# Optimization experiments

Hardware: AMD Instinct MI355X
Metric: run time of the kernel (lower is better)

Reference implementation:

```python
import jax, jax.numpy as jnp
import numpy as np

GRID = (8192, 8192)   # 2D lattice, *dims
NDIM = 2              # links.shape[0]
P_LINK = 0.45         # subcritical bond probability -> finite clusters, bounded step count


def setup_inputs() -> dict:
    key = jax.random.key(0)
    k1, k2 = jax.random.split(key)
    # links[i] marks an open bond between site x and its +1 neighbour along axis i
    links = jax.random.uniform(k1, (NDIM,) + GRID) < P_LINK
    seed_idx = jax.random.randint(k2, (NDIM,), 0, GRID[0]).astype(jnp.int32)
    return {"links": links, "seed_idx": seed_idx}


def _flood_fill(links, seed_idx):
    """Faithful port of ClusterSelection.from_seed_idx: BFS-style roll+mask
    expansion iterated to fixed point via lax.while_loop."""
    ndim = links.shape[0]
    grid = links.shape[1:]
    selected0 = jnp.zeros(grid, dtype=bool).at[tuple(seed_idx)].set(True)

    def cond(carry):
        _, is_done, _ = carry
        return ~is_done

    def body(carry):
        sel0, _, steps = carry
        sel = sel0
        for i in range(ndim):  # unrolled over the (small, static) ndim
            # sites whose -1-neighbour or self is selected can use bond i
            links_to_try = sel0 | jnp.roll(sel0, -1, i)
            links_sel = links_to_try & links[i]
            # a taken bond marks both of its endpoints
            links_sel = links_sel | jnp.roll(links_sel, 1, i)
            sel = sel | links_sel
        is_done = (sel ^ sel0).sum() == 0
        return sel, is_done, steps + 1

    sel, _, steps = jax.lax.while_loop(
        cond, body, (selected0, jnp.array(False), jnp.array(0, jnp.int32))
    )
    return sel, steps


def reference(links, seed_idx):
    sel, _steps = _flood_fill(links, seed_idx)
    return sel
```

## Files before the change

kernel.cpp:

```cpp
#include <hip/hip_runtime.h>
#include <stdint.h>

#define GW 8192
#define GMASK 8191
#define PLANE 67108864ULL
#define TPD 128
#define TMASK 127
#define NTILES 16384
#define QCAP 16384
#define QMASK 16383
#define WPR 128

#define WS_BITMAP 4096
#define WS_TFEVER (WS_BITMAP + 8388608)

#define OUT_U4 16777216u

typedef unsigned long long u64;
typedef unsigned int u32;
typedef unsigned int u32x4 __attribute__((ext_vector_type(4)));

__global__ void clear_bitmap_kernel(uint4* __restrict__ p, int n) {
    int i = blockIdx.x * blockDim.x + threadIdx.x;
    if (i < n) p[i] = make_uint4(0, 0, 0, 0);
}

__device__ __forceinline__ u32 nib4(u32 w) {
    return (((w & 0x01010101u) * 0x01020408u) >> 24) & 0xFu;
}
__device__ __forceinline__ u64 pack_row_b8(const unsigned char* p) {
    const uint4* q = (const uint4*)p;
    u64 w = 0;
#pragma unroll
    for (int i = 0; i < 4; i++) {
        uint4 v = q[i];
        u64 nb = (u64)(nib4(v.x) | (nib4(v.y) << 4) | (nib4(v.z) << 8) | (nib4(v.w) << 12));
        w |= nb << (16 * i);
    }
    return w;
}
__device__ __forceinline__ u64 pack_row_b32(const u32* p) {
    u64 w = 0;
#pragma unroll
    for (int k = 0; k < 16; k++) {
        uint4 v = ((const uint4*)p)[k];
        u64 nb = (u64)((v.x != 0) | ((v.y != 0) << 1) | ((v.z != 0) << 2) | ((v.w != 0) << 3));
        w |= nb << (4 * k);
    }
    return w;
}

__global__ void __launch_bounds__(1024)
mega_kernel(const unsigned char* __restrict__ links8,
            const int* __restrict__ seed_idx,
            unsigned char* __restrict__ ws,
            u32x4* __restrict__ outv) {
    volatile __shared__ unsigned short q[QCAP];
    __shared__ u32 tflags[NTILES / 32];
    __shared__ u32 tfever[NTILES / 32];
    __shared__ int s_qhead, s_qtail, s_active, s_mode, s_c1, s_c3;

    if (blockIdx.x != 0) {
        u32 gtid = (blockIdx.x - 1) * 1024 + threadIdx.x;
        u32 stride = (gridDim.x - 1) * 1024;
        u32x4 z = (u32x4)(0u);
        for (u32 i = gtid; i < OUT_U4; i += stride)
            __builtin_nontemporal_store(z, &outv[i]);
        return;
    }

    u64* bitmap = (u64*)(ws + WS_BITMAP);
    const int tid = threadIdx.x;
    const int ln  = tid & 63;

    for (int i = tid; i < QCAP; i += 1024) q[i] = 0xFFFF;
    for (int i = tid; i < NTILES / 32; i += 1024) { tflags[i] = 0; tfever[i] = 0; }
    if (tid == 0) { s_c1 = 0; s_c3 = 0; s_qhead = 0; s_qtail = 0; s_active = 0; }
    __syncthreads();

    int l1c = 0, l3c = 0;
    for (int i = tid; i < 16384; i += 1024) {
        if (links8[i]) { int m = i & 3; if (m == 1) l1c++; else if (m == 3) l3c++; }
    }
    atomicAdd(&s_c1, l1c);
    atomicAdd(&s_c3, l3c);
    __syncthreads();
    if (tid == 0) {
        s_mode = (s_c1 > 0) ? 0 : ((s_c3 > 0) ? 2 : 1);
        int sr = seed_idx[0] & GMASK, sc = seed_idx[1] & GMASK;
        atomicOr(&bitmap[(u64)sr * WPR + (sc >> 6)], 1ull << (sc & 63));
        int t = (sr >> 6) * TPD + (sc >> 6);
        tflags[t >> 5] = 1u << (t & 31);
        tfever[t >> 5] = 1u << (t & 31);
        q[0] = (unsigned short)t;
        s_qtail = 1; s_active = 1;
    }
    __syncthreads();

    const int mode = s_mode;
    const unsigned char* p0b = links8;
    const unsigned char* p1b = links8 + PLANE;
    const u32* p0w = (const u32*)links8;
    const u32* p1w = (const u32*)(links8 + PLANE * 4);

    auto enq = [&](int t2) {
        u32 bit = 1u << (t2 & 31);
        atomicOr(&tfever[t2 >> 5], bit);
        u32 old = atomicOr(&tflags[t2 >> 5], bit);
        if (!(old & bit)) {
            atomicAdd(&s_active, 1);
            int pos = atomicAdd(&s_qtail, 1) & QMASK;
            q[pos] = (unsigned short)t2;
        }
    };

    long long guard = 0;
    while (true) {
        int t = -1;
        if (ln == 0) {
            while (true) {
                if (*(volatile int*)&s_active == 0) break;
                int h  = *(volatile int*)&s_qhead;
                int tl = *(volatile int*)&s_qtail;
                if (h != tl) {
                    if (atomicCAS(&s_qhead, h, h + 1) == h) {
                        int pos = h & QMASK;
                        unsigned short v;
                        long long g2 = 0;
                        while ((v = q[pos]) == 0xFFFF) { if (++g2 > 400000000LL) break; }
                        q[pos] = 0xFFFF;
                        t = v;
                        break;
                    }
                } else {
                    __builtin_amdgcn_s_sleep(1);
                }
                if (++guard > 400000000LL) break;
            }
        }
        t = __shfl(t, 0);
        if (t < 0) break;

        const int tR = t >> 7, tC = t & TMASK;
        const int c0 = tC * 64;
        if (ln == 0) atomicAnd(&tflags[t >> 5], ~(1u << (t & 31)));
        __threadfence_block();

        const int gr = tR * 64 + ln;
        u64* wp = &bitmap[(u64)gr * WPR + tC];
        u64 loaded = *(volatile u64*)wp;

        u64 l0, l1;
        if (mode == 0) {
            l0 = pack_row_b8(p0b + (u64)gr * GW + tC * 64);
            l1 = pack_row_b8(p1b + (u64)gr * GW + tC * 64);
        } else {
            l0 = pack_row_b32(p0w + (u64)gr * GW + tC * 64);
            l1 = pack_row_b32(p1w + (u64)gr * GW + tC * 64);
        }

        u64 P0 = l1 & 0x7FFFFFFFFFFFFFFFull;
        u64 P1 = P0 & (P0 >> 1);
        u64 P2 = P1 & (P1 >> 2);
        u64 P3 = P2 & (P2 >> 4);
        u64 P4 = P3 & (P3 >> 8);
        u64 P5 = P4 & (P4 >> 16);
        u64 D0 = (ln < 63) ? l0 : 0ull;
        u64 D1 = D0 & __shfl_down(D0, 1);
        u64 D2 = D1 & __shfl_down(D1, 2);
        u64 D3 = D2 & __shfl_down(D2, 4);
        u64 D4 = D3 & __shfl_down(D3, 8);
        u64 D5 = D4 & __shfl_down(D4, 16);

        u64 sel = loaded;
        while (true) {
            u64 old = sel;
            sel |= (sel & P0) << 1;  sel |= (sel >> 1)  & P0;
            sel |= (sel & P1) << 2;  sel |= (sel >> 2)  & P1;
            sel |= (sel & P2) << 4;  sel |= (sel >> 4)  & P2;
            sel |= (sel & P3) << 8;  sel |= (sel >> 8)  & P3;
            sel |= (sel & P4) << 16; sel |= (sel >> 16) & P4;
            sel |= (sel & P5) << 32; sel |= (sel >> 32) & P5;
            sel |= __shfl_up(sel & D0, 1);  sel |= __shfl_down(sel, 1)  & D0;
            sel |= __shfl_up(sel & D1, 2);  sel |= __shfl_down(sel, 2)  & D1;
            sel |= __shfl_up(sel & D2, 4);  sel |= __shfl_down(sel, 4)  & D2;
            sel |= __shfl_up(sel & D3, 8);  sel |= __shfl_down(sel, 8)  & D3;
            sel |= __shfl_up(sel & D4, 16); sel |= __shfl_down(sel, 16) & D4;
            sel |= __shfl_up(sel & D5, 32); sel |= __shfl_down(sel, 32) & D5;
            if (__ballot(sel != old) == 0ull) break;
        }

        u64 newbits = sel & ~loaded;
        if (newbits) atomicOr(wp, newbits);

        bool rnew = false, lnew = false;
        if ((sel >> 63) & (l1 >> 63) & 1ull) {
            u64 old = atomicOr(&bitmap[(u64)gr * WPR + ((tC + 1) & TMASK)], 1ull);
            rnew = !(old & 1ull);
        }
        if (sel & 1ull) {
            u64 lcol2 = (u64)((c0 - 1) & GMASK);
            bool lopen = (mode == 0) ? (p1b[(u64)gr * GW + lcol2] != 0)
                                     : (p1w[(u64)gr * GW + lcol2] != 0);
            if (lopen) {
                u64 old = atomicOr(&bitmap[(u64)gr * WPR + ((tC - 1) & TMASK)], 1ull << 63);
                lnew = !(old & (1ull << 63));
            }
        }
        u64 rmask = __ballot(rnew), lmask = __ballot(lnew);

        const int ga = (tR * 64 - 1) & GMASK;
        u64 top_sel = __shfl(sel, 0);
        u64 umask = 0;
        if (top_sel) {
            bool bopen = ((top_sel >> ln) & 1) &&
                ((mode == 0) ? (p0b[(u64)ga * GW + c0 + ln] != 0)
                             : (p0w[(u64)ga * GW + c0 + ln] != 0));
            umask = __ballot(bopen);
        }
        u64 unew = 0;
        if (ln == 0 && umask) {
            u64 old = atomicOr(&bitmap[(u64)ga * WPR + tC], umask);
            unew = umask & ~old;
        }
        u64 dmask = sel & l0;
        const int gb = (tR * 64 + 64) & GMASK;
        u64 dnew = 0;
        if (ln == 63 && dmask) {
            u64 old = atomicOr(&bitmap[(u64)gb * WPR + tC], dmask);
            dnew = dmask & ~old;
        }

        if (ln == 0  && rmask) enq(tR * TPD + ((tC + 1) & TMASK));
        if (ln == 1  && lmask) enq(tR * TPD + ((tC - 1) & TMASK));
        if (ln == 0  && unew)  enq(((tR - 1) & TMASK) * TPD + tC);
        if (ln == 63 && dnew)  enq(((tR + 1) & TMASK) * TPD + tC);

        if (ln == 0) atomicSub(&s_active, 1);
    }

    __syncthreads();
    for (int i = tid; i < NTILES / 32; i += 1024)
        ((u32*)(ws + WS_TFEVER))[i] = tfever[i];
}

__global__ void __launch_bounds__(256)
writeout_sparse(const unsigned char* __restrict__ ws, u32x4* __restrict__ ob) {
    const u64* bitmap = (const u64*)(ws + WS_BITMAP);
    const u32* tf = (const u32*)(ws + WS_TFEVER);
    for (int t = blockIdx.x; t < NTILES; t += gridDim.x) {
        if (!((tf[t >> 5] >> (t & 31)) & 1u)) continue;
        int tR = t >> 7, tC = t & TMASK;
        for (int i = threadIdx.x; i < 1024; i += 256) {
            int row = i >> 4, c4 = i & 15;
            u64 w = bitmap[(u64)(tR * 64 + row) * WPR + tC];
            u32 nb = (u32)(w >> (c4 * 4)) & 0xFu;
            u32x4 v;
            v.x = nb & 1; v.y = (nb >> 1) & 1; v.z = (nb >> 2) & 1; v.w = (nb >> 3) & 1;
            __builtin_nontemporal_store(
                v, &ob[(u64)(tR * 64 + row) * 2048 + tC * 16 + c4]);
        }
    }
}

extern "C" void kernel_launch(void* const* d_in, const int* in_sizes, int n_in,
                              void* d_out, int out_size, void* d_ws, size_t ws_size,
                              hipStream_t stream) {
    const unsigned char* links = (const unsigned char*)d_in[0];
    const int* seed = (const int*)d_in[1];
    unsigned char* ws = (unsigned char*)d_ws;

    u64* bitmap = (u64*)(ws + WS_BITMAP);

    clear_bitmap_kernel<<<2048, 256, 0, stream>>>((uint4*)bitmap, 524288);
    mega_kernel<<<256, 1024, 0, stream>>>(links, seed, ws, (u32x4*)d_out);
    writeout_sparse<<<1024, 256, 0, stream>>>(ws, (u32x4*)d_out);
}
```

Measured before the change: 658.2 us.

## Fuse sparse writeout into mega kernel with grid-level completion counter

Removes the separate writeout_sparse launch. Block 0 now writes the selected tiles itself after spinning on a global counter that the zero-fill blocks increment once their stores are done. The fill grid doubles to 512 blocks, and the clear kernel now also zeroes the counter word at the start of the workspace. This saves one kernel launch and the tfever round trip through global memory. In exchange, a single block performs the whole writeout, and correctness depends on all fill blocks being co-resident or finishing before block 0 waits on them.

```diff
diff --git a/kernel.cpp b/kernel.cpp
--- a/kernel.cpp
+++ b/kernel.cpp
@@ -12,7 +12,6 @@
 #define WPR 128
 
 #define WS_BITMAP 4096
-#define WS_TFEVER (WS_BITMAP + 8388608)
 
 #define OUT_U4 16777216u
 
@@ -20,9 +19,9 @@
 typedef unsigned int u32;
 typedef unsigned int u32x4 __attribute__((ext_vector_type(4)));
 
-__global__ void clear_bitmap_kernel(uint4* __restrict__ p, int n) {
+__global__ void clear_bitmap_kernel(u32x4* __restrict__ p, int n) {
     int i = blockIdx.x * blockDim.x + threadIdx.x;
-    if (i < n) p[i] = make_uint4(0, 0, 0, 0);
+    if (i < n) p[i] = (u32x4)(0u);
 }
 
 __device__ __forceinline__ u32 nib4(u32 w) {
@@ -60,12 +59,19 @@
     __shared__ u32 tfever[NTILES / 32];
     __shared__ int s_qhead, s_qtail, s_active, s_mode, s_c1, s_c3;
 
+    const u32 nfill = gridDim.x - 1;
+
     if (blockIdx.x != 0) {
         u32 gtid = (blockIdx.x - 1) * 1024 + threadIdx.x;
-        u32 stride = (gridDim.x - 1) * 1024;
+        u32 stride = nfill * 1024;
         u32x4 z = (u32x4)(0u);
         for (u32 i = gtid; i < OUT_U4; i += stride)
             __builtin_nontemporal_store(z, &outv[i]);
+        __syncthreads();
+        if (threadIdx.x == 0) {
+            __threadfence();
+            atomicAdd((u32*)ws, 1u);
+        }
         return;
     }
 
@@ -240,25 +246,24 @@
     }
 
     __syncthreads();
-    for (int i = tid; i < NTILES / 32; i += 1024)
-        ((u32*)(ws + WS_TFEVER))[i] = tfever[i];
-}
-
-__global__ void __launch_bounds__(256)
-writeout_sparse(const unsigned char* __restrict__ ws, u32x4* __restrict__ ob) {
-    const u64* bitmap = (const u64*)(ws + WS_BITMAP);
-    const u32* tf = (const u32*)(ws + WS_TFEVER);
-    for (int t = blockIdx.x; t < NTILES; t += gridDim.x) {
-        if (!((tf[t >> 5] >> (t & 31)) & 1u)) continue;
-        int tR = t >> 7, tC = t & TMASK;
-        for (int i = threadIdx.x; i < 1024; i += 256) {
-            int row = i >> 4, c4 = i & 15;
-            u64 w = bitmap[(u64)(tR * 64 + row) * WPR + tC];
-            u32 nb = (u32)(w >> (c4 * 4)) & 0xFu;
+    if (tid == 0) {
+        while (atomicAdd((u32*)ws, 0u) < nfill) __builtin_amdgcn_s_sleep(8);
+        __threadfence();
+    }
+    __syncthreads();
+
+    for (int wi = 0; wi < NTILES / 32; wi++) {
+        u32 w = tfever[wi];
+        while (w) {
+            int b = __ffs(w) - 1; w &= w - 1;
+            int t = wi * 32 + b;
+            int tR = t >> 7, tC = t & TMASK;
+            int row = tid >> 4, c4 = tid & 15;
+            u64 bmw = bitmap[(u64)(tR * 64 + row) * WPR + tC];
+            u32 nb = (u32)(bmw >> (c4 * 4)) & 0xFu;
             u32x4 v;
             v.x = nb & 1; v.y = (nb >> 1) & 1; v.z = (nb >> 2) & 1; v.w = (nb >> 3) & 1;
-            __builtin_nontemporal_store(
-                v, &ob[(u64)(tR * 64 + row) * 2048 + tC * 16 + c4]);
+            outv[(u64)(tR * 64 + row) * 2048 + tC * 16 + c4] = v;
         }
     }
 }
@@ -270,9 +275,6 @@
     const int* seed = (const int*)d_in[1];
     unsigned char* ws = (unsigned char*)d_ws;
 
-    u64* bitmap = (u64*)(ws + WS_BITMAP);
-
-    clear_bitmap_kernel<<<2048, 256, 0, stream>>>((uint4*)bitmap, 524288);
-    mega_kernel<<<256, 1024, 0, stream>>>(links, seed, ws, (u32x4*)d_out);
-    writeout_sparse<<<1024, 256, 0, stream>>>(ws, (u32x4*)d_out);
-}
+    clear_bitmap_kernel<<<2049, 256, 0, stream>>>((u32x4*)ws, 524544);
+    mega_kernel<<<512, 1024, 0, stream>>>(links, seed, ws, (u32x4*)d_out);
+}
```

After: 695.6 us. 5.7% more time.
